# Kernel tuning notes

Hardware: AMD Instinct MI355X
Metric: run time of the kernel (lower is better)

The kernel has to match this reference:

```python
import jax, jax.numpy as jnp
import numpy as np

DIM = 1024
HEADS = 16
B, N = 2, 2048


def setup_inputs() -> dict:
    key = jax.random.key(0)
    ks = jax.random.split(key, 10)
    s = 1.0 / np.sqrt(DIM)
    return {
        "y2_for": jax.random.normal(ks[0], (B, N, DIM), jnp.float32),
        "y2_back": jax.random.normal(ks[1], (B, N, DIM), jnp.float32),
        "Wq": jax.random.normal(ks[2], (DIM, DIM), jnp.float32) * s,
        "bq": jnp.zeros((DIM,), jnp.float32),
        "Wk": jax.random.normal(ks[3], (DIM, DIM), jnp.float32) * s,
        "bk": jnp.zeros((DIM,), jnp.float32),
        "Wv": jax.random.normal(ks[4], (DIM, DIM), jnp.float32) * s,
        "bv": jnp.zeros((DIM,), jnp.float32),
        "Wo": jax.random.normal(ks[5], (DIM, DIM), jnp.float32) * s,
        "bo": jnp.zeros((DIM,), jnp.float32),
    }


def reference(y2_for, y2_back, Wq, bq, Wk, bk, Wv, bv, Wo, bo):
    h = HEADS
    d = DIM // h
    scale = d ** -0.5
    q = y2_for @ Wq + bq                    # [b, n, dim]
    k = y2_back @ Wk + bk
    v = (y2_back + y2_for) @ Wv + bv

    def split_heads(x):
        b, n, _ = x.shape
        return x.reshape(b, n, h, d).transpose(0, 2, 1, 3)  # [b, h, n, d]

    q, k, v = split_heads(q), split_heads(k), split_heads(v)
    attn = jax.nn.softmax(jnp.einsum('bhid,bhjd->bhij', q, k) * scale, axis=-1)
    out = jnp.einsum('bhij,bhjd->bhid', attn, v)
    out = out.transpose(0, 2, 1, 3).reshape(y2_for.shape)   # [b, n, dim]
    out = out + y2_for + y2_back
    return out @ Wo + bo
```

## Files before the change

### kernel.cpp

```cpp
#include <hip/hip_runtime.h>

#define DIM 1024
#define HEADS 16
#define BB 2
#define NN 2048
#define HD 64
#define M_ROWS (BB*NN)

typedef __bf16 bf16x8 __attribute__((ext_vector_type(8)));
typedef float f32x4 __attribute__((ext_vector_type(4)));
typedef short s16x4 __attribute__((ext_vector_type(4)));

__device__ inline unsigned short f2bf(float f) {
    unsigned int u = __builtin_bit_cast(unsigned int, f);
    u += 0x7fffu + ((u >> 16) & 1u);
    return (unsigned short)(u >> 16);
}
__device__ inline float bf2f(unsigned short u) {
    return __builtin_bit_cast(float, (unsigned int)u << 16);
}
__device__ inline bf16x8 as_bf16x8(uint4 v) {
    return __builtin_bit_cast(bf16x8, v);
}
__device__ __forceinline__ void gl_lds16(const unsigned short* g, unsigned short* l) {
    __builtin_amdgcn_global_load_lds(
        (const __attribute__((address_space(1))) unsigned int*)g,
        (__attribute__((address_space(3))) unsigned int*)l, 16, 0, 0);
}

__device__ __forceinline__ f32x4 mfma16x16x16bf16(s16x4 a, s16x4 b, f32x4 c) {
#if __has_builtin(__builtin_amdgcn_mfma_f32_16x16x16bf16_1k)
    return __builtin_amdgcn_mfma_f32_16x16x16bf16_1k(a, b, c, 0, 0, 0);
#else
    asm volatile("v_mfma_f32_16x16x16_bf16 %0, %1, %2, %0"
                 : "+v"(c) : "v"(a), "v"(b));
    return c;
#endif
}

__global__ __launch_bounds__(256) void prep_w(
    const float* __restrict__ Wq, const float* __restrict__ Wk,
    const float* __restrict__ Wv, const float* __restrict__ Wo,
    unsigned short* __restrict__ Wt_all)
{
    __shared__ float tile[32][33];
    const int m = blockIdx.z;
    const float* W = (m == 0) ? Wq : (m == 1) ? Wk : (m == 2) ? Wv : Wo;
    const int bk = blockIdx.x, bn = blockIdx.y;
    const int tx = threadIdx.x & 31, ty = threadIdx.x >> 5;

    #pragma unroll
    for (int i = 0; i < 32; i += 8)
        tile[ty + i][tx] = W[(size_t)(bk*32 + ty + i)*DIM + bn*32 + tx];
    __syncthreads();
    unsigned short* dst = Wt_all + (size_t)m * DIM * DIM;
    #pragma unroll
    for (int i = 0; i < 32; i += 8)
        dst[(size_t)(bn*32 + ty + i)*DIM + bk*32 + tx] = f2bf(tile[tx][ty + i]);
}

__global__ __launch_bounds__(256) void prep_act(
    const float* __restrict__ y2f, const float* __restrict__ y2b,
    unsigned short* __restrict__ Af, unsigned short* __restrict__ Ab,
    unsigned short* __restrict__ As)
{
    const size_t idx = ((size_t)blockIdx.x*256 + threadIdx.x) * 8;
    #pragma unroll
    for (int half = 0; half < 2; half++) {
        float4 f = *(const float4*)(y2f + idx + half*4);
        float4 b = *(const float4*)(y2b + idx + half*4);
        ushort4 of, ob, os;
        of.x = f2bf(f.x); of.y = f2bf(f.y); of.z = f2bf(f.z); of.w = f2bf(f.w);
        ob.x = f2bf(b.x); ob.y = f2bf(b.y); ob.z = f2bf(b.z); ob.w = f2bf(b.w);
        os.x = f2bf(f.x + b.x); os.y = f2bf(f.y + b.y);
        os.z = f2bf(f.z + b.z); os.w = f2bf(f.w + b.w);
        *(ushort4*)(Af + idx + half*4) = of;
        *(ushort4*)(Ab + idx + half*4) = ob;
        *(ushort4*)(As + idx + half*4) = os;
    }
}

__global__ __launch_bounds__(256) void gemm_qkv(
    const unsigned short* __restrict__ Af, const unsigned short* __restrict__ Ab,
    const unsigned short* __restrict__ As,
    const unsigned short* __restrict__ Wt_all,
    const float* __restrict__ bq, const float* __restrict__ bk,
    const float* __restrict__ bv,
    unsigned short* __restrict__ Qh, unsigned short* __restrict__ Kh,
    unsigned short* __restrict__ Vt)
{
    const int bm = blockIdx.x;
    const int mode = blockIdx.y >> 3;
    const int bn = blockIdx.y & 7;
    __shared__ __align__(16) unsigned short smem[8192];
    unsigned short* sA = smem;
    unsigned short* sB = smem + 4096;
    const int t = threadIdx.x;
    const int w = t >> 6, lane = t & 63, ln = lane & 15, quad = lane >> 4;
    const int wm = w >> 1, wn = w & 1;
    const unsigned short* Wt = Wt_all + (size_t)mode * (DIM*DIM);
    const unsigned short* A0 = (mode == 0) ? Af : (mode == 1) ? Ab : As;

    const int srow = lane >> 2;
    const int scol = (lane & 3) * 8;

    f32x4 acc[4][4];
    #pragma unroll
    for (int mi = 0; mi < 4; mi++)
        #pragma unroll
        for (int ni = 0; ni < 4; ni++)
            acc[mi][ni] = (f32x4){0.f, 0.f, 0.f, 0.f};

    for (int kt = 0; kt < 32; kt++) {
        __syncthreads();
        #pragma unroll
        for (int j = 0; j < 2; j++) {
            int row = w*32 + j*16;
            gl_lds16(A0 + (size_t)(bm*128 + row + srow)*DIM + kt*32 + scol,
                     &sA[row*32]);
            gl_lds16(Wt + (size_t)(bn*128 + row + srow)*DIM + kt*32 + scol,
                     &sB[row*32]);
        }
        __syncthreads();

        bf16x8 af[4], bfr[4];
        #pragma unroll
        for (int mi = 0; mi < 4; mi++)
            af[mi] = as_bf16x8(*(const uint4*)(&sA[(wm*64 + mi*16 + ln)*32 + quad*8]));
        #pragma unroll
        for (int ni = 0; ni < 4; ni++)
            bfr[ni] = as_bf16x8(*(const uint4*)(&sB[(wn*64 + ni*16 + ln)*32 + quad*8]));
        #pragma unroll
        for (int mi = 0; mi < 4; mi++)
            #pragma unroll
            for (int ni = 0; ni < 4; ni++)
                acc[mi][ni] = __builtin_amdgcn_mfma_f32_16x16x32_bf16(af[mi], bfr[ni], acc[mi][ni], 0, 0, 0);
    }

    const float* bias = (mode == 0) ? bq : (mode == 1) ? bk : bv;
    unsigned short* dst = (mode == 0) ? Qh : (mode == 1) ? Kh : Vt;
    if (mode < 2) {
        const float sc = (mode == 0) ? 0.125f * 1.4426950408889634f : 1.0f;
        #pragma unroll
        for (int mi = 0; mi < 4; mi++) {
            #pragma unroll
            for (int r = 0; r < 4; r++) {
                int grow = bm*128 + wm*64 + mi*16 + quad*4 + r;
                int b_ = grow >> 11, n = grow & (NN - 1);
                #pragma unroll
                for (int ni = 0; ni < 4; ni++) {
                    int gcol = bn*128 + wn*64 + ni*16 + ln;
                    int hh = gcol >> 6, dd = gcol & 63;
                    float val = (acc[mi][ni][r] + bias[gcol]) * sc;
                    dst[(((size_t)(b_*HEADS + hh))*NN + n)*HD + dd] = f2bf(val);
                }
            }
        }
    } else {
        #pragma unroll
        for (int p = 0; p < 2; p++) {
            __syncthreads();
            if (wn == p) {
                #pragma unroll
                for (int mi = 0; mi < 4; mi++)
                    #pragma unroll
                    for (int ni = 0; ni < 4; ni++) {
                        float bsv = bias[bn*128 + wn*64 + ni*16 + ln];
                        ushort4 pk;
                        pk.x = f2bf(acc[mi][ni][0] + bsv);
                        pk.y = f2bf(acc[mi][ni][1] + bsv);
                        pk.z = f2bf(acc[mi][ni][2] + bsv);
                        pk.w = f2bf(acc[mi][ni][3] + bsv);
                        *(ushort4*)(&smem[(ni*16 + ln)*128 + wm*64 + mi*16 + quad*4]) = pk;
                    }
            }
            __syncthreads();
            const int hh = bn*2 + p, b_ = bm >> 4;
            unsigned short* vrow = dst + (((size_t)(b_*HEADS + hh))*HD)*NN
                                       + (size_t)(bm & 15)*128;
            #pragma unroll
            for (int i = 0; i < 4; i++) {
                int idx = i*256 + t;
                int dd = idx >> 4, ch = (idx & 15)*8;
                *(uint4*)(vrow + (size_t)dd*NN + ch) = *(const uint4*)(&smem[dd*128 + ch]);
            }
        }
    }
}

__global__ __launch_bounds__(256) void gemm_out(
    const unsigned short* __restrict__ attp,
    const unsigned short* __restrict__ Wt_all,
    const float* __restrict__ bo, float* __restrict__ out)
{
    const int bm = blockIdx.x, bn = blockIdx.y;
    __shared__ __align__(16) unsigned short sA[64*32];
    __shared__ __align__(16) unsigned short sB[128*32];
    const int t = threadIdx.x;
    const int w = t >> 6, lane = t & 63, ln = lane & 15, quad = lane >> 4;
    const int wm = w >> 1, wn = w & 1;
    const unsigned short* Wt = Wt_all + (size_t)3 * (DIM*DIM);

    const int srow = lane >> 2;
    const int scol = (lane & 3) * 8;

    f32x4 acc[2][4];
    #pragma unroll
    for (int mi = 0; mi < 2; mi++)
        #pragma unroll
        for (int ni = 0; ni < 4; ni++)
            acc[mi][ni] = (f32x4){0.f, 0.f, 0.f, 0.f};

    for (int kt = 0; kt < 32; kt++) {
        __syncthreads();
        gl_lds16(attp + (size_t)(bm*64 + w*16 + srow)*DIM + kt*32 + scol,
                 &sA[(w*16)*32]);
        #pragma unroll
        for (int j = 0; j < 2; j++) {
            int row = w*32 + j*16;
            gl_lds16(Wt + (size_t)(bn*128 + row + srow)*DIM + kt*32 + scol,
                     &sB[row*32]);
        }
        __syncthreads();

        bf16x8 af[2], bfr[4];
        #pragma unroll
        for (int mi = 0; mi < 2; mi++)
            af[mi] = as_bf16x8(*(const uint4*)(&sA[(wm*32 + mi*16 + ln)*32 + quad*8]));
        #pragma unroll
        for (int ni = 0; ni < 4; ni++)
            bfr[ni] = as_bf16x8(*(const uint4*)(&sB[(wn*64 + ni*16 + ln)*32 + quad*8]));
        #pragma unroll
        for (int mi = 0; mi < 2; mi++)
            #pragma unroll
            for (int ni = 0; ni < 4; ni++)
                acc[mi][ni] = __builtin_amdgcn_mfma_f32_16x16x32_bf16(af[mi], bfr[ni], acc[mi][ni], 0, 0, 0);
    }

    #pragma unroll
    for (int mi = 0; mi < 2; mi++) {
        #pragma unroll
        for (int r = 0; r < 4; r++) {
            int grow = bm*64 + wm*32 + mi*16 + quad*4 + r;
            #pragma unroll
            for (int ni = 0; ni < 4; ni++) {
                int gcol = bn*128 + wn*64 + ni*16 + ln;
                out[(size_t)grow*DIM + gcol] = acc[mi][ni][r] + bo[gcol];
            }
        }
    }
}

__global__ __launch_bounds__(256) void attn_kernel(
    const unsigned short* __restrict__ Qh, const unsigned short* __restrict__ Kh,
    const unsigned short* __restrict__ Vt, const unsigned short* __restrict__ As,
    unsigned short* __restrict__ attp)
{
    const int bh = blockIdx.x;
    const int qt = blockIdx.y;
    const int b = bh >> 4, h = bh & 15;
    const int t = threadIdx.x;
    const int w = t >> 6, lane = t & 63, ln = lane & 15, quad = lane >> 4;
    const int sw = ln & 7;
    const float EBIAS = 17.312340490667562f;

    __shared__ __align__(16) unsigned short sK[2][64*64];
    __shared__ __align__(16) unsigned short sVt[2][64*64];

    const unsigned short* Qb  = Qh + (size_t)bh * NN * HD + (size_t)qt * 64 * HD;
    const unsigned short* Kb  = Kh + (size_t)bh * NN * HD;
    const unsigned short* Vtb = Vt + (size_t)bh * HD * NN;

    const int rl = lane >> 3, cb = lane & 7;

    bf16x8 aq[2];
    #pragma unroll
    for (int k = 0; k < 2; k++)
        aq[k] = as_bf16x8(*(const uint4*)(Qb + (size_t)(w*16 + ln)*HD + (k*4 + quad)*8));

#define STAGE_KV(JT, BBUF) do { \
        _Pragma("unroll") \
        for (int j = 0; j < 2; j++) { \
            int row = w*16 + j*8 + rl; \
            gl_lds16(Kb + (size_t)((JT)*64 + row)*HD + ((cb ^ (row & 7))*8), \
                     &sK[BBUF][(w*16 + j*8)*64]); \
            gl_lds16(Vtb + (size_t)row*NN + (JT)*64 + ((cb ^ (row & 7))*8), \
                     &sVt[BBUF][(w*16 + j*8)*64]); \
        } } while (0)

    const s16x4 ones = { (short)0x3F80, (short)0x3F80, (short)0x3F80, (short)0x3F80 };
    f32x4 accO[4], accL;
    accL = (f32x4){0.f, 0.f, 0.f, 0.f};
    #pragma unroll
    for (int di = 0; di < 4; di++) accO[di] = (f32x4){0.f, 0.f, 0.f, 0.f};

    STAGE_KV(0, 0);

    #pragma unroll 2
    for (int jt = 0; jt < 32; jt++) {
        const int cur = jt & 1;
        if (jt < 31) {
            STAGE_KV(jt + 1, cur ^ 1);
            asm volatile("s_waitcnt vmcnt(4)" ::: "memory");
        } else {
            asm volatile("s_waitcnt vmcnt(0)" ::: "memory");
        }
        __builtin_amdgcn_s_barrier();
        __builtin_amdgcn_sched_barrier(0);

        const unsigned short* sKc = sK[cur];
        const unsigned short* sVc = sVt[cur];

        f32x4 accS[4];
        #pragma unroll
        for (int ni = 0; ni < 4; ni++)
            accS[ni] = (f32x4){-EBIAS, -EBIAS, -EBIAS, -EBIAS};
        __builtin_amdgcn_s_setprio(1);
        #pragma unroll
        for (int ni = 0; ni < 4; ni++)
            #pragma unroll
            for (int k = 0; k < 2; k++) {
                bf16x8 bkf = as_bf16x8(*(const uint4*)(
                    &sKc[(ni*16 + ln)*64 + (((k*4 + quad) ^ sw)*8)]));
                accS[ni] = __builtin_amdgcn_mfma_f32_16x16x32_bf16(bkf, aq[k], accS[ni], 0, 0, 0);
            }
        __builtin_amdgcn_s_setprio(0);

        s16x4 pf[4];
        #pragma unroll
        for (int ni = 0; ni < 4; ni++) {
            unsigned int e0 = __builtin_bit_cast(unsigned int, __builtin_amdgcn_exp2f(accS[ni][0]));
            unsigned int e1 = __builtin_bit_cast(unsigned int, __builtin_amdgcn_exp2f(accS[ni][1]));
            unsigned int e2 = __builtin_bit_cast(unsigned int, __builtin_amdgcn_exp2f(accS[ni][2]));
            unsigned int e3 = __builtin_bit_cast(unsigned int, __builtin_amdgcn_exp2f(accS[ni][3]));
            unsigned int lo = __builtin_amdgcn_perm(e1, e0, 0x07060302u);
            unsigned int hi = __builtin_amdgcn_perm(e3, e2, 0x07060302u);
            pf[ni] = __builtin_bit_cast(s16x4, uint2{lo, hi});
            accL = mfma16x16x16bf16(pf[ni], ones, accL);
        }

        __builtin_amdgcn_s_setprio(1);
        #pragma unroll
        for (int ni = 0; ni < 4; ni++) {
            int blkv = 2*ni + (quad >> 1);
            int off = (quad & 1) * 4;
            #pragma unroll
            for (int di = 0; di < 4; di++) {
                s16x4 bv = __builtin_bit_cast(s16x4,
                    *(const uint2*)(&sVc[(di*16 + ln)*64 + ((blkv ^ sw)*8) + off]));
                accO[di] = mfma16x16x16bf16(pf[ni], bv, accO[di]);
            }
        }
        __builtin_amdgcn_s_setprio(0);

        __builtin_amdgcn_sched_barrier(0);
        __builtin_amdgcn_s_barrier();
    }
#undef STAGE_KV

    #pragma unroll
    for (int r = 0; r < 4; r++) {
        float inv = 1.f / accL[r];
        int n = qt*64 + w*16 + quad*4 + r;
        #pragma unroll
        for (int di = 0; di < 4; di++) {
            int c = h*64 + di*16 + ln;
            size_t gi = ((size_t)b*NN + n)*DIM + c;
            float o = accO[di][r]*inv + bf2f(As[gi]);
            attp[gi] = f2bf(o);
        }
    }
}

extern "C" void kernel_launch(void* const* d_in, const int* in_sizes, int n_in,
                              void* d_out, int out_size, void* d_ws, size_t ws_size,
                              hipStream_t stream) {
    const float* y2f = (const float*)d_in[0];
    const float* y2b = (const float*)d_in[1];
    const float* Wq  = (const float*)d_in[2];
    const float* bq  = (const float*)d_in[3];
    const float* Wk  = (const float*)d_in[4];
    const float* bk  = (const float*)d_in[5];
    const float* Wv  = (const float*)d_in[6];
    const float* bv  = (const float*)d_in[7];
    const float* Wo  = (const float*)d_in[8];
    const float* bo  = (const float*)d_in[9];
    float* out = (float*)d_out;

    const size_t NACT = (size_t)M_ROWS * DIM;
    unsigned short* ws   = (unsigned short*)d_ws;
    unsigned short* Af   = ws;
    unsigned short* Ab   = ws + NACT;
    unsigned short* As   = ws + 2*NACT;
    unsigned short* Qh   = ws + 3*NACT;
    unsigned short* Kh   = ws + 4*NACT;
    unsigned short* Vt   = ws + 5*NACT;
    unsigned short* Wt   = ws + 6*NACT;
    unsigned short* attp = Ab;

    prep_w<<<dim3(32, 32, 4), 256, 0, stream>>>(Wq, Wk, Wv, Wo, Wt);
    prep_act<<<dim3(2048), 256, 0, stream>>>(y2f, y2b, Af, Ab, As);
    gemm_qkv<<<dim3(32, 24), 256, 0, stream>>>(
        Af, Ab, As, Wt, bq, bk, bv, Qh, Kh, Vt);
    attn_kernel<<<dim3(32, 32), 256, 0, stream>>>(Qh, Kh, Vt, As, attp);
    gemm_out<<<dim3(64, 8), 256, 0, stream>>>(attp, Wt, bo, out);
}
```

Measured before the change: 242.8 us.

## Double-buffer LDS in both GEMMs and restructure attention barrier placement

Adds double-buffered LDS staging to the QKV and output GEMMs, so the next k-tile's global-to-LDS load is issued before the current tile's MFMAs and waited on only at the end of the iteration, replacing two syncthreads per step with one barrier. The attention loop is changed to the same single-barrier-per-iteration pattern, waiting on loads at the end of the iteration instead of the start. The V-transpose epilogue now writes all 128 columns at once through a swizzled LDS layout to avoid bank conflicts, dropping the two-pass loop. LDS use doubles, which may lower occupancy.

```diff
diff --git a/kernel.cpp b/kernel.cpp
--- a/kernel.cpp
+++ b/kernel.cpp
@@ -92,9 +92,7 @@
     const int bm = blockIdx.x;
     const int mode = blockIdx.y >> 3;
     const int bn = blockIdx.y & 7;
-    __shared__ __align__(16) unsigned short smem[8192];
-    unsigned short* sA = smem;
-    unsigned short* sB = smem + 4096;
+    __shared__ __align__(16) unsigned short smem[16384];
     const int t = threadIdx.x;
     const int w = t >> 6, lane = t & 63, ln = lane & 15, quad = lane >> 4;
     const int wm = w >> 1, wn = w & 1;
@@ -111,31 +109,50 @@
         for (int ni = 0; ni < 4; ni++)
             acc[mi][ni] = (f32x4){0.f, 0.f, 0.f, 0.f};
 
+#define STAGE_G(KT, BUF) do { \
+        unsigned short* sa_ = smem + (BUF)*8192; \
+        _Pragma("unroll") \
+        for (int j = 0; j < 2; j++) { \
+            int row = w*32 + j*16; \
+            gl_lds16(A0 + (size_t)(bm*128 + row + srow)*DIM + (KT)*32 + scol, \
+                     &sa_[row*32]); \
+            gl_lds16(Wt + (size_t)(bn*128 + row + srow)*DIM + (KT)*32 + scol, \
+                     &sa_[4096 + row*32]); \
+        } } while (0)
+
+    STAGE_G(0, 0);
+    asm volatile("s_waitcnt vmcnt(0)" ::: "memory");
+    __builtin_amdgcn_s_barrier();
+    __builtin_amdgcn_sched_barrier(0);
+
+    #pragma unroll 2
     for (int kt = 0; kt < 32; kt++) {
-        __syncthreads();
-        #pragma unroll
-        for (int j = 0; j < 2; j++) {
-            int row = w*32 + j*16;
-            gl_lds16(A0 + (size_t)(bm*128 + row + srow)*DIM + kt*32 + scol,
-                     &sA[row*32]);
-            gl_lds16(Wt + (size_t)(bn*128 + row + srow)*DIM + kt*32 + scol,
-                     &sB[row*32]);
-        }
-        __syncthreads();
-
+        const int cur = kt & 1;
+        if (kt < 31) STAGE_G(kt + 1, cur ^ 1);
+
+        const unsigned short* sa = smem + cur*8192;
+        const unsigned short* sb = sa + 4096;
         bf16x8 af[4], bfr[4];
         #pragma unroll
         for (int mi = 0; mi < 4; mi++)
-            af[mi] = as_bf16x8(*(const uint4*)(&sA[(wm*64 + mi*16 + ln)*32 + quad*8]));
-        #pragma unroll
-        for (int ni = 0; ni < 4; ni++)
-            bfr[ni] = as_bf16x8(*(const uint4*)(&sB[(wn*64 + ni*16 + ln)*32 + quad*8]));
+            af[mi] = as_bf16x8(*(const uint4*)(&sa[(wm*64 + mi*16 + ln)*32 + quad*8]));
+        #pragma unroll
+        for (int ni = 0; ni < 4; ni++)
+            bfr[ni] = as_bf16x8(*(const uint4*)(&sb[(wn*64 + ni*16 + ln)*32 + quad*8]));
         #pragma unroll
         for (int mi = 0; mi < 4; mi++)
             #pragma unroll
             for (int ni = 0; ni < 4; ni++)
                 acc[mi][ni] = __builtin_amdgcn_mfma_f32_16x16x32_bf16(af[mi], bfr[ni], acc[mi][ni], 0, 0, 0);
-    }
+
+        __builtin_amdgcn_sched_barrier(0);
+        if (kt < 31) {
+            asm volatile("s_waitcnt vmcnt(0)" ::: "memory");
+            __builtin_amdgcn_s_barrier();
+            __builtin_amdgcn_sched_barrier(0);
+        }
+    }
+#undef STAGE_G
 
     const float* bias = (mode == 0) ? bq : (mode == 1) ? bk : bv;
     unsigned short* dst = (mode == 0) ? Qh : (mode == 1) ? Kh : Vt;
@@ -157,33 +174,34 @@
             }
         }
     } else {
-        #pragma unroll
-        for (int p = 0; p < 2; p++) {
-            __syncthreads();
-            if (wn == p) {
-                #pragma unroll
-                for (int mi = 0; mi < 4; mi++)
-                    #pragma unroll
-                    for (int ni = 0; ni < 4; ni++) {
-                        float bsv = bias[bn*128 + wn*64 + ni*16 + ln];
-                        ushort4 pk;
-                        pk.x = f2bf(acc[mi][ni][0] + bsv);
-                        pk.y = f2bf(acc[mi][ni][1] + bsv);
-                        pk.z = f2bf(acc[mi][ni][2] + bsv);
-                        pk.w = f2bf(acc[mi][ni][3] + bsv);
-                        *(ushort4*)(&smem[(ni*16 + ln)*128 + wm*64 + mi*16 + quad*4]) = pk;
-                    }
+        __syncthreads();
+        #pragma unroll
+        for (int ni = 0; ni < 4; ni++) {
+            int row_s = wn*64 + ni*16 + ln;
+            float bsv = bias[bn*128 + row_s];
+            int sxor = (row_s & 7) << 1;
+            #pragma unroll
+            for (int mi = 0; mi < 4; mi++) {
+                int u = wm*16 + mi*4 + quad;
+                ushort4 pk;
+                pk.x = f2bf(acc[mi][ni][0] + bsv);
+                pk.y = f2bf(acc[mi][ni][1] + bsv);
+                pk.z = f2bf(acc[mi][ni][2] + bsv);
+                pk.w = f2bf(acc[mi][ni][3] + bsv);
+                *(ushort4*)(&smem[row_s*128 + ((u ^ sxor) << 2)]) = pk;
             }
-            __syncthreads();
-            const int hh = bn*2 + p, b_ = bm >> 4;
-            unsigned short* vrow = dst + (((size_t)(b_*HEADS + hh))*HD)*NN
-                                       + (size_t)(bm & 15)*128;
-            #pragma unroll
-            for (int i = 0; i < 4; i++) {
-                int idx = i*256 + t;
-                int dd = idx >> 4, ch = (idx & 15)*8;
-                *(uint4*)(vrow + (size_t)dd*NN + ch) = *(const uint4*)(&smem[dd*128 + ch]);
-            }
+        }
+        __syncthreads();
+        const int b_ = bm >> 4;
+        #pragma unroll
+        for (int i = 0; i < 8; i++) {
+            int idx = i*256 + t;
+            int dd = idx >> 4, jc = idx & 15;
+            int u = (jc*2) ^ ((dd & 7) << 1);
+            int hh = bn*2 + (dd >> 6), d_ = dd & 63;
+            *(uint4*)(dst + (((size_t)(b_*HEADS + hh))*HD + d_)*NN
+                          + (size_t)(bm & 15)*128 + jc*8)
+                = *(const uint4*)(&smem[dd*128 + (u << 2)]);
         }
     }
 }
@@ -194,8 +212,7 @@
     const float* __restrict__ bo, float* __restrict__ out)
 {
     const int bm = blockIdx.x, bn = blockIdx.y;
-    __shared__ __align__(16) unsigned short sA[64*32];
-    __shared__ __align__(16) unsigned short sB[128*32];
+    __shared__ __align__(16) unsigned short smem[12288];
     const int t = threadIdx.x;
     const int w = t >> 6, lane = t & 63, ln = lane & 15, quad = lane >> 4;
     const int wm = w >> 1, wn = w & 1;
@@ -211,31 +228,50 @@
         for (int ni = 0; ni < 4; ni++)
             acc[mi][ni] = (f32x4){0.f, 0.f, 0.f, 0.f};
 
+#define STAGE_O(KT, BUF) do { \
+        unsigned short* sa_ = smem + (BUF)*6144; \
+        gl_lds16(attp + (size_t)(bm*64 + w*16 + srow)*DIM + (KT)*32 + scol, \
+                 &sa_[(w*16)*32]); \
+        _Pragma("unroll") \
+        for (int j = 0; j < 2; j++) { \
+            int row = w*32 + j*16; \
+            gl_lds16(Wt + (size_t)(bn*128 + row + srow)*DIM + (KT)*32 + scol, \
+                     &sa_[2048 + row*32]); \
+        } } while (0)
+
+    STAGE_O(0, 0);
+    asm volatile("s_waitcnt vmcnt(0)" ::: "memory");
+    __builtin_amdgcn_s_barrier();
+    __builtin_amdgcn_sched_barrier(0);
+
+    #pragma unroll 2
     for (int kt = 0; kt < 32; kt++) {
-        __syncthreads();
-        gl_lds16(attp + (size_t)(bm*64 + w*16 + srow)*DIM + kt*32 + scol,
-                 &sA[(w*16)*32]);
-        #pragma unroll
-        for (int j = 0; j < 2; j++) {
-            int row = w*32 + j*16;
-            gl_lds16(Wt + (size_t)(bn*128 + row + srow)*DIM + kt*32 + scol,
-                     &sB[row*32]);
-        }
-        __syncthreads();
-
+        const int cur = kt & 1;
+        if (kt < 31) STAGE_O(kt + 1, cur ^ 1);
+
+        const unsigned short* sa = smem + cur*6144;
+        const unsigned short* sb = sa + 2048;
         bf16x8 af[2], bfr[4];
         #pragma unroll
         for (int mi = 0; mi < 2; mi++)
-            af[mi] = as_bf16x8(*(const uint4*)(&sA[(wm*32 + mi*16 + ln)*32 + quad*8]));
-        #pragma unroll
-        for (int ni = 0; ni < 4; ni++)
-            bfr[ni] = as_bf16x8(*(const uint4*)(&sB[(wn*64 + ni*16 + ln)*32 + quad*8]));
+            af[mi] = as_bf16x8(*(const uint4*)(&sa[(wm*32 + mi*16 + ln)*32 + quad*8]));
+        #pragma unroll
+        for (int ni = 0; ni < 4; ni++)
+            bfr[ni] = as_bf16x8(*(const uint4*)(&sb[(wn*64 + ni*16 + ln)*32 + quad*8]));
         #pragma unroll
         for (int mi = 0; mi < 2; mi++)
             #pragma unroll
             for (int ni = 0; ni < 4; ni++)
                 acc[mi][ni] = __builtin_amdgcn_mfma_f32_16x16x32_bf16(af[mi], bfr[ni], acc[mi][ni], 0, 0, 0);
-    }
+
+        __builtin_amdgcn_sched_barrier(0);
+        if (kt < 31) {
+            asm volatile("s_waitcnt vmcnt(0)" ::: "memory");
+            __builtin_amdgcn_s_barrier();
+            __builtin_amdgcn_sched_barrier(0);
+        }
+    }
+#undef STAGE_O
 
     #pragma unroll
     for (int mi = 0; mi < 2; mi++) {
@@ -295,18 +331,14 @@
     for (int di = 0; di < 4; di++) accO[di] = (f32x4){0.f, 0.f, 0.f, 0.f};
 
     STAGE_KV(0, 0);
+    asm volatile("s_waitcnt vmcnt(0)" ::: "memory");
+    __builtin_amdgcn_s_barrier();
+    __builtin_amdgcn_sched_barrier(0);
 
     #pragma unroll 2
     for (int jt = 0; jt < 32; jt++) {
         const int cur = jt & 1;
-        if (jt < 31) {
-            STAGE_KV(jt + 1, cur ^ 1);
-            asm volatile("s_waitcnt vmcnt(4)" ::: "memory");
-        } else {
-            asm volatile("s_waitcnt vmcnt(0)" ::: "memory");
-        }
-        __builtin_amdgcn_s_barrier();
-        __builtin_amdgcn_sched_barrier(0);
+        if (jt < 31) STAGE_KV(jt + 1, cur ^ 1);
 
         const unsigned short* sKc = sK[cur];
         const unsigned short* sVc = sVt[cur];
@@ -354,7 +386,11 @@
         __builtin_amdgcn_s_setprio(0);
 
         __builtin_amdgcn_sched_barrier(0);
-        __builtin_amdgcn_s_barrier();
+        if (jt < 31) {
+            asm volatile("s_waitcnt vmcnt(0)" ::: "memory");
+            __builtin_amdgcn_s_barrier();
+            __builtin_amdgcn_sched_barrier(0);
+        }
     }
 #undef STAGE_KV
 
```

After: 227.4 us. 1.07x faster.
